# Kernel optimization log

Measured on AMD Instinct MI355X. Metric: run time of the kernel, lower is better.

Reference implementation:

```python
import jax, jax.numpy as jnp
import numpy as np
import math

N = 30000        # nodes
E = 390000       # edges (first N are self-loops, in node order)
H = 64
NNS = 4          # num_node_states
NES = 4          # num_edge_states
NGRAPH = 64      # graphs in batch
TEMP_ON_EVAL = 1.0


def from_binary(bits):
    # bits: [..., k] of {0,1} -> integer code sum(bits * 2^k)
    pw = (2 ** jnp.arange(bits.shape[-1])).astype(bits.dtype)
    return jnp.sum(bits * pw, axis=-1)


def segment_softmax(logits, seg, num_seg, tau):
    m = jax.ops.segment_max(logits, seg, num_segments=num_seg)
    e = jnp.exp((logits - m[seg]) / tau)
    s = jax.ops.segment_sum(e, seg, num_segments=num_seg)
    return e / s[seg]


def segment_hard_onehot(logits, seg, num_seg):
    # gumbel_softmax with tau=0, no noise: one-hot at per-segment argmax (first on ties)
    n = logits.shape[0]
    m = jax.ops.segment_max(logits, seg, num_segments=num_seg)
    idx = jnp.where(logits >= m[seg], jnp.arange(n, dtype=jnp.int32), jnp.int32(n))
    first = jax.ops.segment_min(idx, seg, num_segments=num_seg)
    return (jnp.arange(n, dtype=jnp.int32) == first[seg]).astype(jnp.int32)


def select_best(emb, bits, scalars, index, num_index):
    # SelectBest with use_select_best=True. states are even ints < 2^(k+1);
    # unique((states, index)) groups == fused key states*num_index+index.
    states = 2 * from_binary(bits)
    key = states * num_index + index
    num_key = (2 ** (bits.shape[-1] + 1)) * num_index
    best = segment_hard_onehot(-scalars[:, 0], key, num_key)
    return emb[states + best]


def temp_by_step(step, upper, lower, num_iter, temp_on_eval):
    if step == -1:
        return temp_on_eval
    frac = min(float(step) / num_iter, 1.0)
    return upper + (lower - upper) * frac


def forward(node_states, edge_states, scalars, edge_index, batch_vec, rev_idx,
            emb_edge, emb_sbv, emb_sbr, emb_static,
            Wq, Wk, Wv, Wek, Wev, Wc, training_step):
    ei0, ei1 = edge_index[0], edge_index[1]
    # self-loop edges are the first N edges in node order ->
    # scalars[edge_index[0]==edge_index[1]] == scalars[:N]
    node_scalars = scalars[:N]                                   # [N,1]

    # select_best_from_virtual
    node_fts = select_best(emb_sbv, node_states, node_scalars, batch_vec, NGRAPH)  # [N,H]
    edge_fts = emb_edge[from_binary(edge_states)]                # [E,H]

    Q = node_fts @ Wq.T
    K = node_fts @ Wk.T
    V = node_fts @ Wv.T

    # combined_edge_KV
    sb = select_best(emb_sbr, node_states[ei0], scalars, ei1, N)  # [E,H]
    edge_K = sb @ Wek.T
    sender_s = node_scalars[ei0]                                  # [E,1]
    reciever_s = node_scalars[ei1]                                # [E,1]
    rlx = (scalars < reciever_s)
    rlx_d = (sender_s + scalars < reciever_s)
    fts = jnp.concatenate([rlx, rlx_d], axis=-1).astype(jnp.int32)  # [E,2] bits
    static_fts = emb_static[from_binary(fts)]                     # [E,H]
    combined = jnp.concatenate([edge_fts, edge_fts[rev_idx], static_fts], axis=1)  # [E,3H]
    edge_V = combined @ Wc.T                                      # [E,H]

    # compute_message
    Qe = Q[ei1]
    Ke = K[ei0] + edge_K
    Ve = V[ei0] + edge_V
    alpha = jnp.sum(Qe * Ke, axis=-1) / math.sqrt(H)              # [E]
    tau = temp_by_step(int(training_step), 3.0, 0.1, 10000, TEMP_ON_EVAL)
    alpha = segment_softmax(alpha, ei1, N, tau)
    message = Ve * alpha[:, None]                                  # [E,H]

    node_out = node_fts + jax.ops.segment_sum(message, ei1, num_segments=N)
    edge_out = edge_fts + message
    return node_out, edge_out


def setup_inputs() -> dict:
    key = jax.random.key(0)
    ks = jax.random.split(key, 16)
    node_states = jax.random.randint(ks[0], (N, NNS), 0, 2, dtype=jnp.int32)
    edge_states = jax.random.randint(ks[1], (E, NES), 0, 2, dtype=jnp.int32)
    scalars = jax.random.normal(ks[2], (E, 1), dtype=jnp.float32)
    loops = jnp.arange(N, dtype=jnp.int32)
    senders = jax.random.randint(ks[3], (E - N,), 0, N, dtype=jnp.int32)
    receivers = jax.random.randint(ks[4], (E - N,), 0, N, dtype=jnp.int32)
    edge_index = jnp.stack([jnp.concatenate([loops, senders]),
                            jnp.concatenate([loops, receivers])])  # [2,E]
    batch_vec = jnp.sort(jax.random.randint(ks[5], (N,), 0, NGRAPH, dtype=jnp.int32))
    rev_idx = jax.random.permutation(ks[6], E).astype(jnp.int32)
    s = 0.05
    return {
        'node_states': node_states, 'edge_states': edge_states, 'scalars': scalars,
        'edge_index': edge_index, 'batch_vec': batch_vec, 'rev_idx': rev_idx,
        'emb_edge': s * jax.random.normal(ks[7], (2 ** NES, H), dtype=jnp.float32),
        'emb_sbv': s * jax.random.normal(ks[8], (2 ** (NNS + 1), H), dtype=jnp.float32),
        'emb_sbr': s * jax.random.normal(ks[9], (2 ** (NNS + 1), H), dtype=jnp.float32),
        'emb_static': s * jax.random.normal(ks[10], (4, H), dtype=jnp.float32),
        'Wq': s * jax.random.normal(ks[11], (H, H), dtype=jnp.float32),
        'Wk': s * jax.random.normal(ks[12], (H, H), dtype=jnp.float32),
        'Wv': s * jax.random.normal(ks[13], (H, H), dtype=jnp.float32),
        'Wek': s * jax.random.normal(ks[14], (H, H), dtype=jnp.float32),
        'Wev': s * jax.random.normal(ks[15], (H, H), dtype=jnp.float32),
        'Wc': s * jax.random.normal(jax.random.fold_in(key, 99), (H, 3 * H), dtype=jnp.float32),
        'training_step': -1,
    }


def reference(node_states, edge_states, scalars, edge_index, batch_vec, rev_idx,
              emb_edge, emb_sbv, emb_sbr, emb_static,
              Wq, Wk, Wv, Wek, Wev, Wc, training_step):
    return forward(node_states, edge_states, scalars, edge_index, batch_vec, rev_idx,
                   emb_edge, emb_sbv, emb_sbr, emb_static,
                   Wq, Wk, Wv, Wek, Wev, Wc, training_step)
```

## Files before the change

kernel.cpp:

```cpp
#include <hip/hip_runtime.h>

#define NN 30000
#define NE 390000
#define HH 64
#define NGRAPH 64
#define AGG_BLOCKS 1024
#define NE_BLK 1524
#define NN_BLK 118

__device__ __forceinline__ unsigned sortable_f32(float f) {
    unsigned u = __float_as_uint(f);
    return (u & 0x80000000u) ? ~u : (u | 0x80000000u);
}

#define T_V   0
#define T_C1  2048
#define T_C2  3072
#define T_C3  4096
#define T_A   4352
#define T_B   5376
#define T_Q   6400
#define T_K   8448
#define T_EK  10496

__global__ __launch_bounds__(256) void k_init(
        const int4* __restrict__ edge_states, const int4* __restrict__ node_states,
        const float* __restrict__ emb_sbv, const float* __restrict__ emb_sbr,
        const float* __restrict__ emb_edge, const float* __restrict__ emb_static,
        const float* __restrict__ Wq, const float* __restrict__ Wk,
        const float* __restrict__ Wv, const float* __restrict__ Wek,
        const float* __restrict__ Wc,
        unsigned char* __restrict__ esi, int* __restrict__ ns,
        unsigned* __restrict__ cnt, unsigned long long* __restrict__ nodeSel,
        float* __restrict__ tabs) {
    int b = blockIdx.x, t = threadIdx.x;
    if (b < NE_BLK) {
        int e = b * 256 + t;
        if (e < NE) {
            int4 v = edge_states[e];
            esi[e] = (unsigned char)(v.x + 2*v.y + 4*v.z + 8*v.w);
        }
    } else if (b < NE_BLK + NN_BLK) {
        int i = (b - NE_BLK) * 256 + t;
        if (i < NN) {
            int4 v = node_states[i];
            ns[i] = 2 * (v.x + 2*v.y + 4*v.z + 8*v.w);
            cnt[i] = 0u;
        }
    } else if (b < NE_BLK + NN_BLK + 41) {
        int idx = (b - NE_BLK - NN_BLK) * 256 + t;
        if (idx >= 10496) return;
        float acc = 0.f;
        if (idx < 2048) {
            int r = idx >> 6, h = idx & 63;
            for (int j = 0; j < 64; ++j) acc += emb_sbv[r*64+j] * Wv[h*64+j];
            tabs[T_V + idx] = acc;
        } else if (idx < 3072) {
            int x = idx - 2048; int r = x >> 6, h = x & 63;
            for (int j = 0; j < 64; ++j) acc += emb_edge[r*64+j] * Wc[h*192+j];
            tabs[T_C1 + x] = acc;
        } else if (idx < 4096) {
            int x = idx - 3072; int r = x >> 6, h = x & 63;
            for (int j = 0; j < 64; ++j) acc += emb_edge[r*64+j] * Wc[h*192+64+j];
            tabs[T_C2 + x] = acc;
        } else if (idx < 4352) {
            int x = idx - 4096; int r = x >> 6, h = x & 63;
            for (int j = 0; j < 64; ++j) acc += emb_static[r*64+j] * Wc[h*192+128+j];
            tabs[T_C3 + x] = acc;
        } else if (idx < 6400) {
            int x = idx - 4352; int r = x >> 6, h = x & 63;
            for (int j = 0; j < 64; ++j) acc += emb_sbv[r*64+j] * Wq[h*64+j];
            tabs[T_Q + x] = acc;
        } else if (idx < 8448) {
            int x = idx - 6400; int r = x >> 6, h = x & 63;
            for (int j = 0; j < 64; ++j) acc += emb_sbv[r*64+j] * Wk[h*64+j];
            tabs[T_K + x] = acc;
        } else {
            int x = idx - 8448; int r = x >> 6, h = x & 63;
            for (int j = 0; j < 64; ++j) acc += emb_sbr[r*64+j] * Wek[h*64+j];
            tabs[T_EK + x] = acc;
        }
    } else {
        #pragma unroll
        for (int k = 0; k < 4; ++k) nodeSel[t * 4 + k] = ~0ull;
    }
}

__global__ __launch_bounds__(256) void k_phase2(
        const int* __restrict__ ei1, unsigned* __restrict__ cnt,
        unsigned* __restrict__ rank, const int* __restrict__ ns,
        const int* __restrict__ batch_vec, const float* __restrict__ scalars,
        unsigned long long* __restrict__ nodeSel, float* __restrict__ tabs) {
    int b = blockIdx.x, t = threadIdx.x;
    if (b < NE_BLK) {
        int e = b * 256 + t;
        if (e < NE) rank[e] = atomicAdd(&cnt[ei1[e]], 1u);
    } else if (b < NE_BLK + NN_BLK) {
        int i = (b - NE_BLK) * 256 + t;
        if (i < NN) {
            int st = ns[i];
            int key = (st >> 1) * NGRAPH + batch_vec[i];
            unsigned long long pk = ((unsigned long long)sortable_f32(scalars[i]) << 32) | (unsigned)i;
            atomicMin(&nodeSel[key], pk);
        }
    } else {
        int idx = (b - NE_BLK - NN_BLK) * 256 + t;
        if (idx >= 2048) return;
        const float* TQ = tabs + T_Q;
        float acc = 0.f;
        if (idx < 1024) {
            int r1 = idx >> 5, r0 = idx & 31;
            const float* TK = tabs + T_K;
            for (int j = 0; j < 64; ++j) acc += TQ[r1*64+j] * TK[r0*64+j];
            tabs[T_A + idx] = acc * 0.125f;
        } else {
            int x = idx - 1024; int r1 = x >> 5, rk = x & 31;
            const float* TEK = tabs + T_EK;
            for (int j = 0; j < 64; ++j) acc += TQ[r1*64+j] * TEK[rk*64+j];
            tabs[T_B + x] = acc * 0.125f;
        }
    }
}

__global__ __launch_bounds__(256) void k_phase3(
        const unsigned* __restrict__ cnt, unsigned* __restrict__ bsum,
        const int* __restrict__ ns, const int* __restrict__ batch_vec,
        const unsigned long long* __restrict__ nodeSel,
        const float* __restrict__ scalars, uint2* __restrict__ nodePk) {
    int b = blockIdx.x, t = threadIdx.x;
    if (b < NN_BLK) {
        __shared__ unsigned red[256];
        int i = b * 256 + t;
        red[t] = (i < NN) ? cnt[i] : 0u;
        __syncthreads();
        for (int o = 128; o > 0; o >>= 1) {
            if (t < o) red[t] += red[t + o];
            __syncthreads();
        }
        if (t == 0) bsum[b] = red[0];
    } else {
        int i = (b - NN_BLK) * 256 + t;
        if (i < NN) {
            int st = ns[i];
            int key = (st >> 1) * NGRAPH + batch_vec[i];
            unsigned win = (unsigned)(nodeSel[key] & 0xffffffffull);
            unsigned row = (unsigned)st + (win == (unsigned)i ? 1u : 0u);
            nodePk[i] = make_uint2(row, __float_as_uint(scalars[i]));
        }
    }
}

__global__ __launch_bounds__(128) void k_sscan(const unsigned* __restrict__ bsum,
                                               unsigned* __restrict__ bbase,
                                               unsigned* __restrict__ base) {
    __shared__ unsigned s[128];
    int t = threadIdx.x;
    unsigned v = (t < NN_BLK) ? bsum[t] : 0u;
    s[t] = v;
    __syncthreads();
    for (int o = 1; o < 128; o <<= 1) {
        unsigned u = (t >= o) ? s[t - o] : 0u;
        __syncthreads();
        s[t] += u;
        __syncthreads();
    }
    if (t < NN_BLK) bbase[t] = s[t] - v;
    if (t == 127) { bbase[NN_BLK] = s[127]; base[NN] = s[127]; }
}

__global__ __launch_bounds__(256) void k_base(const unsigned* __restrict__ cnt,
        const unsigned* __restrict__ bbase, unsigned* __restrict__ base) {
    __shared__ unsigned s[256];
    int t = threadIdx.x;
    int i = blockIdx.x * 256 + t;
    unsigned v = (i < NN) ? cnt[i] : 0u;
    s[t] = v;
    __syncthreads();
    for (int o = 1; o < 256; o <<= 1) {
        unsigned u = (t >= o) ? s[t - o] : 0u;
        __syncthreads();
        s[t] += u;
        __syncthreads();
    }
    if (i < NN) base[i] = bbase[blockIdx.x] + s[t] - v;
}

__global__ __launch_bounds__(256) void k_edge2(const int* __restrict__ ei0,
        const int* __restrict__ ei1, const uint2* __restrict__ nodePk,
        const unsigned char* __restrict__ esi, const int* __restrict__ rev_idx,
        const float* __restrict__ scalars, const unsigned* __restrict__ base,
        const unsigned* __restrict__ rank, uint2* __restrict__ sKey,
        float* __restrict__ sScal) {
    int e = blockIdx.x * 256 + threadIdx.x;
    if (e >= NE) return;
    int s0 = ei0[e], s1 = ei1[e];
    uint2 np = nodePk[s0];
    unsigned es = esi[e];
    unsigned esr = esi[rev_idx[e]];
    unsigned pos = base[s1] + rank[e];
    sKey[pos] = make_uint2((unsigned)e | (np.x << 19) | (es << 24) | (esr << 28), np.y);
    sScal[pos] = scalars[e];
}

__global__ __launch_bounds__(256) void k_agg(
        const unsigned* __restrict__ base, const uint2* __restrict__ sKey,
        const float* __restrict__ sScal, const uint2* __restrict__ nodePk,
        const float* __restrict__ tabs, const float* __restrict__ emb_edge,
        const float* __restrict__ emb_sbv, const int* __restrict__ step_ptr,
        float* __restrict__ out_node, float* __restrict__ out_edge) {
    __shared__ float lds[9472];
    __shared__ unsigned scr[4][32];
    int tid = threadIdx.x;
    for (int j = tid; j < 6400; j += 256) lds[j] = tabs[j];
    for (int j = tid; j < 1024; j += 256) lds[6400 + j] = emb_edge[j];
    for (int j = tid; j < 2048; j += 256) lds[7424 + j] = emb_sbv[j];
    __syncthreads();
    int step = step_ptr[0];
    float invTau;
    if (step == -1) invTau = 1.0f;
    else { float frac = fminf((float)step / 10000.f, 1.f); invTau = 1.0f / (3.0f + (0.1f - 3.0f) * frac); }
    int wid = tid >> 6, lane = tid & 63;
    unsigned* mySc = scr[wid];
    unsigned* myE  = scr[wid] + 16;
    int q = lane >> 4, cidx = (lane & 15) << 2;
    for (int i = blockIdx.x * 4 + wid; i < NN; i += AGG_BLOCKS * 4) {
        unsigned j0 = base[i], j1 = base[i + 1];
        int d = (int)(j1 - j0);
        uint2 np = nodePk[i];
        int r1 = (int)np.x;
        float recv = __uint_as_float(np.y);
        const float* Arow = lds + T_A + r1 * 32;
        const float* Brow = lds + T_B + r1 * 32;
        float4 acc = {0.f, 0.f, 0.f, 0.f};
        if (lane < 16) { mySc[lane] = 0xffffffffu; myE[lane] = 0xffffffffu; }
        __builtin_amdgcn_sched_barrier(0);
        if (d > 0 && d <= 64) {
            bool act = lane < d;
            uint2 key = act ? sKey[j0 + lane] : make_uint2(0u, 0u);
            float sc  = act ? sScal[j0 + lane] : 0.f;
            unsigned scs = sortable_f32(sc);
            unsigned g = (key.x >> 20) & 15u;
            unsigned e19 = key.x & 0x7ffffu;
            if (act) atomicMin(&mySc[g], scs);
            __builtin_amdgcn_sched_barrier(0);
            unsigned ms = mySc[g];
            if (act && scs == ms) atomicMin(&myE[g], e19);
            __builtin_amdgcn_sched_barrier(0);
            bool win = act && (myE[g] == e19);
            int r0 = (key.x >> 19) & 31;
            int ekrow = (r0 & 30) + (win ? 1 : 0);
            float ex = act ? __expf((Arow[r0] + Brow[ekrow]) * invTau) : 0.f;
            float send = __uint_as_float(key.y);
            int si = (sc < recv ? 1 : 0) + (send + sc < recv ? 2 : 0);
            float s = ex;
            #pragma unroll
            for (int o = 1; o < 64; o <<= 1) s += __shfl_xor(s, o);
            float p = ex / s;
            int nIt = (d + 3) >> 2;
            for (int it = 0; it < nIt; ++it) {
                int jj = it * 4 + q;
                unsigned kx = __shfl(key.x, jj);
                int sii = __shfl(si, jj);
                float pp = __shfl(p, jj);
                if (jj < d) {
                    unsigned e = kx & 0x7ffffu;
                    int rr0 = (kx >> 19) & 31, es = (kx >> 24) & 15, esr = (kx >> 28) & 15;
                    float4 tv = *(const float4*)&lds[(rr0 << 6) + cidx];
                    float4 c1 = *(const float4*)&lds[T_C1 + (es << 6) + cidx];
                    float4 c2 = *(const float4*)&lds[T_C2 + (esr << 6) + cidx];
                    float4 c3 = *(const float4*)&lds[T_C3 + (sii << 6) + cidx];
                    float4 ee = *(const float4*)&lds[6400 + (es << 6) + cidx];
                    float4 o;
                    o.x = pp * (tv.x + c1.x + c2.x + c3.x);
                    o.y = pp * (tv.y + c1.y + c2.y + c3.y);
                    o.z = pp * (tv.z + c1.z + c2.z + c3.z);
                    o.w = pp * (tv.w + c1.w + c2.w + c3.w);
                    acc.x += o.x; acc.y += o.y; acc.z += o.z; acc.w += o.w;
                    o.x += ee.x; o.y += ee.y; o.z += ee.z; o.w += ee.w;
                    *(float4*)&out_edge[(size_t)e * 64 + cidx] = o;
                }
            }
        } else if (d > 64) {
            for (unsigned c = j0; c < j1; c += 64) {
                unsigned j = c + lane;
                if (j < j1) {
                    uint2 key = sKey[j];
                    atomicMin(&mySc[(key.x >> 20) & 15u], sortable_f32(sScal[j]));
                }
            }
            __builtin_amdgcn_sched_barrier(0);
            for (unsigned c = j0; c < j1; c += 64) {
                unsigned j = c + lane;
                if (j < j1) {
                    uint2 key = sKey[j];
                    unsigned g = (key.x >> 20) & 15u;
                    if (sortable_f32(sScal[j]) == mySc[g]) atomicMin(&myE[g], key.x & 0x7ffffu);
                }
            }
            __builtin_amdgcn_sched_barrier(0);
            float s = 0.f;
            for (unsigned c = j0; c < j1; c += 64) {
                unsigned j = c + lane;
                if (j < j1) {
                    uint2 key = sKey[j];
                    bool win = (myE[(key.x >> 20) & 15u] == (key.x & 0x7ffffu));
                    int r0 = (key.x >> 19) & 31;
                    int ekrow = (r0 & 30) + (win ? 1 : 0);
                    s += __expf((Arow[r0] + Brow[ekrow]) * invTau);
                }
            }
            #pragma unroll
            for (int o = 1; o < 64; o <<= 1) s += __shfl_xor(s, o);
            float invS = 1.f / s;
            for (unsigned c = j0; c < j1; c += 4) {
                unsigned j = c + q;
                if (j < j1) {
                    uint2 key = sKey[j];
                    float sc = sScal[j];
                    bool win = (myE[(key.x >> 20) & 15u] == (key.x & 0x7ffffu));
                    int r0 = (key.x >> 19) & 31;
                    int ekrow = (r0 & 30) + (win ? 1 : 0);
                    float pp = __expf((Arow[r0] + Brow[ekrow]) * invTau) * invS;
                    float send = __uint_as_float(key.y);
                    int si = (sc < recv ? 1 : 0) + (send + sc < recv ? 2 : 0);
                    unsigned e = key.x & 0x7ffffu;
                    int es = (key.x >> 24) & 15, esr = (key.x >> 28) & 15;
                    float4 tv = *(const float4*)&lds[(r0 << 6) + cidx];
                    float4 c1 = *(const float4*)&lds[T_C1 + (es << 6) + cidx];
                    float4 c2 = *(const float4*)&lds[T_C2 + (esr << 6) + cidx];
                    float4 c3 = *(const float4*)&lds[T_C3 + (si << 6) + cidx];
                    float4 ee = *(const float4*)&lds[6400 + (es << 6) + cidx];
                    float4 o;
                    o.x = pp * (tv.x + c1.x + c2.x + c3.x);
                    o.y = pp * (tv.y + c1.y + c2.y + c3.y);
                    o.z = pp * (tv.z + c1.z + c2.z + c3.z);
                    o.w = pp * (tv.w + c1.w + c2.w + c3.w);
                    acc.x += o.x; acc.y += o.y; acc.z += o.z; acc.w += o.w;
                    o.x += ee.x; o.y += ee.y; o.z += ee.z; o.w += ee.w;
                    *(float4*)&out_edge[(size_t)e * 64 + cidx] = o;
                }
            }
        }
        acc.x += __shfl_xor(acc.x, 16); acc.y += __shfl_xor(acc.y, 16);
        acc.z += __shfl_xor(acc.z, 16); acc.w += __shfl_xor(acc.w, 16);
        acc.x += __shfl_xor(acc.x, 32); acc.y += __shfl_xor(acc.y, 32);
        acc.z += __shfl_xor(acc.z, 32); acc.w += __shfl_xor(acc.w, 32);
        if (lane < 16) {
            float4 nb = *(const float4*)&lds[7424 + (r1 << 6) + cidx];
            float4 o;
            o.x = nb.x + acc.x; o.y = nb.y + acc.y; o.z = nb.z + acc.z; o.w = nb.w + acc.w;
            *(float4*)&out_node[(size_t)i * 64 + cidx] = o;
        }
    }
}

extern "C" void kernel_launch(void* const* d_in, const int* in_sizes, int n_in,
                              void* d_out, int out_size, void* d_ws, size_t ws_size,
                              hipStream_t stream) {
    const int4*  node_states = (const int4*)d_in[0];
    const int4*  edge_states = (const int4*)d_in[1];
    const float* scalars     = (const float*)d_in[2];
    const int*   edge_index  = (const int*)d_in[3];
    const int*   batch_vec   = (const int*)d_in[4];
    const int*   rev_idx     = (const int*)d_in[5];
    const float* emb_edge    = (const float*)d_in[6];
    const float* emb_sbv     = (const float*)d_in[7];
    const float* emb_sbr     = (const float*)d_in[8];
    const float* emb_static  = (const float*)d_in[9];
    const float* Wq  = (const float*)d_in[10];
    const float* Wk  = (const float*)d_in[11];
    const float* Wv  = (const float*)d_in[12];
    const float* Wek = (const float*)d_in[13];
    const float* Wc  = (const float*)d_in[15];
    const int*   step = (const int*)d_in[16];

    const int* ei0 = edge_index;
    const int* ei1 = edge_index + NE;

    char* ws = (char*)d_ws;
    int*      ns     = (int*)(ws);
    uint2*    nodePk = (uint2*)(ws + 120000);
    unsigned char* esi = (unsigned char*)(ws + 360000);
    unsigned* rank   = (unsigned*)(ws + 750016);
    unsigned* cnt    = (unsigned*)(ws + 2310016);
    unsigned* baseA  = (unsigned*)(ws + 2430080);
    uint2*    sKey   = (uint2*)(ws + 2550144);
    float*    sScal  = (float*)(ws + 5670144);
    unsigned long long* nodeSel = (unsigned long long*)(ws + 7230144);
    float*    tabs   = (float*)(ws + 7238336);
    unsigned* bsum   = (unsigned*)(ws + 7288512);
    unsigned* bbase  = (unsigned*)(ws + 7289024);

    float* out_node = (float*)d_out;
    float* out_edge = out_node + (size_t)NN * HH;

    hipLaunchKernelGGL(k_init, dim3(NE_BLK + NN_BLK + 41 + 1), dim3(256), 0, stream,
                       edge_states, node_states, emb_sbv, emb_sbr, emb_edge, emb_static,
                       Wq, Wk, Wv, Wek, Wc, esi, ns, cnt, nodeSel, tabs);
    hipLaunchKernelGGL(k_phase2, dim3(NE_BLK + NN_BLK + 8), dim3(256), 0, stream,
                       ei1, cnt, rank, ns, batch_vec, scalars, nodeSel, tabs);
    hipLaunchKernelGGL(k_phase3, dim3(NN_BLK * 2), dim3(256), 0, stream,
                       cnt, bsum, ns, batch_vec, nodeSel, scalars, nodePk);
    hipLaunchKernelGGL(k_sscan, dim3(1), dim3(128), 0, stream, bsum, bbase, baseA);
    hipLaunchKernelGGL(k_base, dim3(NN_BLK), dim3(256), 0, stream, cnt, bbase, baseA);
    hipLaunchKernelGGL(k_edge2, dim3(NE_BLK), dim3(256), 0, stream,
                       ei0, ei1, nodePk, esi, rev_idx, scalars, baseA, rank, sKey, sScal);
    hipLaunchKernelGGL(k_agg, dim3(AGG_BLOCKS), dim3(256), 0, stream,
                       baseA, sKey, sScal, nodePk, tabs, emb_edge, emb_sbv, step,
                       out_node, out_edge);
}
```

Before: 77.44 us.

## Fuse CSR scan kernels, pack edge payload, single 64-bit argmin atomic

Replaces the three-kernel block-sum/scan/base pipeline with one kernel in which each block recomputes its own prefix by summing all earlier counts, removing two launches. Edge key, sender scalar and edge scalar are packed into one 16-byte record, so aggregation issues one load per edge. The two-pass per-group argmin (min scalar, then min edge id) becomes a single 64-bit atomicMin on a packed (scalar, id) value. emb_sbv is read from global memory instead of LDS to shrink shared memory, and the aggregation grid grows. The trade-off is redundant prefix reads in later scan blocks and a wider payload with a padding word.

```diff
diff --git a/kernel.cpp b/kernel.cpp
--- a/kernel.cpp
+++ b/kernel.cpp
@@ -4,7 +4,7 @@
 #define NE 390000
 #define HH 64
 #define NGRAPH 64
-#define AGG_BLOCKS 1024
+#define AGG_BLOCKS 1536
 #define NE_BLK 1524
 #define NN_BLK 118
 
@@ -122,22 +122,37 @@
     }
 }
 
-__global__ __launch_bounds__(256) void k_phase3(
-        const unsigned* __restrict__ cnt, unsigned* __restrict__ bsum,
+__global__ __launch_bounds__(256) void k_csr(
+        const unsigned* __restrict__ cnt, unsigned* __restrict__ base,
         const int* __restrict__ ns, const int* __restrict__ batch_vec,
         const unsigned long long* __restrict__ nodeSel,
         const float* __restrict__ scalars, uint2* __restrict__ nodePk) {
     int b = blockIdx.x, t = threadIdx.x;
     if (b < NN_BLK) {
         __shared__ unsigned red[256];
-        int i = b * 256 + t;
-        red[t] = (i < NN) ? cnt[i] : 0u;
+        __shared__ unsigned sc[256];
+        unsigned pre = 0;
+        int lim = b * 256;
+        for (int j = t; j < lim; j += 256) pre += cnt[j];
+        red[t] = pre;
         __syncthreads();
         for (int o = 128; o > 0; o >>= 1) {
             if (t < o) red[t] += red[t + o];
             __syncthreads();
         }
-        if (t == 0) bsum[b] = red[0];
+        unsigned P = red[0];
+        int i = lim + t;
+        unsigned v = (i < NN) ? cnt[i] : 0u;
+        sc[t] = v;
+        __syncthreads();
+        for (int o = 1; o < 256; o <<= 1) {
+            unsigned u = (t >= o) ? sc[t - o] : 0u;
+            __syncthreads();
+            sc[t] += u;
+            __syncthreads();
+        }
+        if (i < NN) base[i] = P + sc[t] - v;
+        if (b == NN_BLK - 1 && t == 255) base[NN] = P + sc[255];
     } else {
         int i = (b - NN_BLK) * 256 + t;
         if (i < NN) {
@@ -150,47 +165,11 @@
     }
 }
 
-__global__ __launch_bounds__(128) void k_sscan(const unsigned* __restrict__ bsum,
-                                               unsigned* __restrict__ bbase,
-                                               unsigned* __restrict__ base) {
-    __shared__ unsigned s[128];
-    int t = threadIdx.x;
-    unsigned v = (t < NN_BLK) ? bsum[t] : 0u;
-    s[t] = v;
-    __syncthreads();
-    for (int o = 1; o < 128; o <<= 1) {
-        unsigned u = (t >= o) ? s[t - o] : 0u;
-        __syncthreads();
-        s[t] += u;
-        __syncthreads();
-    }
-    if (t < NN_BLK) bbase[t] = s[t] - v;
-    if (t == 127) { bbase[NN_BLK] = s[127]; base[NN] = s[127]; }
-}
-
-__global__ __launch_bounds__(256) void k_base(const unsigned* __restrict__ cnt,
-        const unsigned* __restrict__ bbase, unsigned* __restrict__ base) {
-    __shared__ unsigned s[256];
-    int t = threadIdx.x;
-    int i = blockIdx.x * 256 + t;
-    unsigned v = (i < NN) ? cnt[i] : 0u;
-    s[t] = v;
-    __syncthreads();
-    for (int o = 1; o < 256; o <<= 1) {
-        unsigned u = (t >= o) ? s[t - o] : 0u;
-        __syncthreads();
-        s[t] += u;
-        __syncthreads();
-    }
-    if (i < NN) base[i] = bbase[blockIdx.x] + s[t] - v;
-}
-
 __global__ __launch_bounds__(256) void k_edge2(const int* __restrict__ ei0,
         const int* __restrict__ ei1, const uint2* __restrict__ nodePk,
         const unsigned char* __restrict__ esi, const int* __restrict__ rev_idx,
         const float* __restrict__ scalars, const unsigned* __restrict__ base,
-        const unsigned* __restrict__ rank, uint2* __restrict__ sKey,
-        float* __restrict__ sScal) {
+        const unsigned* __restrict__ rank, uint4* __restrict__ sPay) {
     int e = blockIdx.x * 256 + threadIdx.x;
     if (e >= NE) return;
     int s0 = ei0[e], s1 = ei1[e];
@@ -198,30 +177,28 @@
     unsigned es = esi[e];
     unsigned esr = esi[rev_idx[e]];
     unsigned pos = base[s1] + rank[e];
-    sKey[pos] = make_uint2((unsigned)e | (np.x << 19) | (es << 24) | (esr << 28), np.y);
-    sScal[pos] = scalars[e];
+    sPay[pos] = make_uint4((unsigned)e | (np.x << 19) | (es << 24) | (esr << 28),
+                           np.y, __float_as_uint(scalars[e]), 0u);
 }
 
 __global__ __launch_bounds__(256) void k_agg(
-        const unsigned* __restrict__ base, const uint2* __restrict__ sKey,
-        const float* __restrict__ sScal, const uint2* __restrict__ nodePk,
-        const float* __restrict__ tabs, const float* __restrict__ emb_edge,
-        const float* __restrict__ emb_sbv, const int* __restrict__ step_ptr,
+        const unsigned* __restrict__ base, const uint4* __restrict__ sPay,
+        const uint2* __restrict__ nodePk, const float* __restrict__ tabs,
+        const float* __restrict__ emb_edge, const float* __restrict__ emb_sbv,
+        const int* __restrict__ step_ptr,
         float* __restrict__ out_node, float* __restrict__ out_edge) {
-    __shared__ float lds[9472];
-    __shared__ unsigned scr[4][32];
+    __shared__ float lds[7424];
+    __shared__ unsigned long long scr[4][16];
     int tid = threadIdx.x;
     for (int j = tid; j < 6400; j += 256) lds[j] = tabs[j];
     for (int j = tid; j < 1024; j += 256) lds[6400 + j] = emb_edge[j];
-    for (int j = tid; j < 2048; j += 256) lds[7424 + j] = emb_sbv[j];
     __syncthreads();
     int step = step_ptr[0];
     float invTau;
     if (step == -1) invTau = 1.0f;
     else { float frac = fminf((float)step / 10000.f, 1.f); invTau = 1.0f / (3.0f + (0.1f - 3.0f) * frac); }
     int wid = tid >> 6, lane = tid & 63;
-    unsigned* mySc = scr[wid];
-    unsigned* myE  = scr[wid] + 16;
+    unsigned long long* myPk = scr[wid];
     int q = lane >> 4, cidx = (lane & 15) << 2;
     for (int i = blockIdx.x * 4 + wid; i < NN; i += AGG_BLOCKS * 4) {
         unsigned j0 = base[i], j1 = base[i + 1];
@@ -232,25 +209,22 @@
         const float* Arow = lds + T_A + r1 * 32;
         const float* Brow = lds + T_B + r1 * 32;
         float4 acc = {0.f, 0.f, 0.f, 0.f};
-        if (lane < 16) { mySc[lane] = 0xffffffffu; myE[lane] = 0xffffffffu; }
+        if (lane < 16) myPk[lane] = ~0ull;
         __builtin_amdgcn_sched_barrier(0);
         if (d > 0 && d <= 64) {
             bool act = lane < d;
-            uint2 key = act ? sKey[j0 + lane] : make_uint2(0u, 0u);
-            float sc  = act ? sScal[j0 + lane] : 0.f;
-            unsigned scs = sortable_f32(sc);
-            unsigned g = (key.x >> 20) & 15u;
-            unsigned e19 = key.x & 0x7ffffu;
-            if (act) atomicMin(&mySc[g], scs);
+            uint4 pay = act ? sPay[j0 + lane] : make_uint4(0u, 0u, 0u, 0u);
+            float sc  = __uint_as_float(pay.z);
+            unsigned g = (pay.x >> 20) & 15u;
+            unsigned e19 = pay.x & 0x7ffffu;
+            unsigned long long pk = ((unsigned long long)sortable_f32(sc) << 32) | e19;
+            if (act) atomicMin(&myPk[g], pk);
             __builtin_amdgcn_sched_barrier(0);
-            unsigned ms = mySc[g];
-            if (act && scs == ms) atomicMin(&myE[g], e19);
-            __builtin_amdgcn_sched_barrier(0);
-            bool win = act && (myE[g] == e19);
-            int r0 = (key.x >> 19) & 31;
+            bool win = act && (myPk[g] == pk);
+            int r0 = (pay.x >> 19) & 31;
             int ekrow = (r0 & 30) + (win ? 1 : 0);
             float ex = act ? __expf((Arow[r0] + Brow[ekrow]) * invTau) : 0.f;
-            float send = __uint_as_float(key.y);
+            float send = __uint_as_float(pay.y);
             int si = (sc < recv ? 1 : 0) + (send + sc < recv ? 2 : 0);
             float s = ex;
             #pragma unroll
@@ -259,7 +233,7 @@
             int nIt = (d + 3) >> 2;
             for (int it = 0; it < nIt; ++it) {
                 int jj = it * 4 + q;
-                unsigned kx = __shfl(key.x, jj);
+                unsigned kx = __shfl(pay.x, jj);
                 int sii = __shfl(si, jj);
                 float pp = __shfl(p, jj);
                 if (jj < d) {
@@ -284,17 +258,11 @@
             for (unsigned c = j0; c < j1; c += 64) {
                 unsigned j = c + lane;
                 if (j < j1) {
-                    uint2 key = sKey[j];
-                    atomicMin(&mySc[(key.x >> 20) & 15u], sortable_f32(sScal[j]));
-                }
-            }
-            __builtin_amdgcn_sched_barrier(0);
-            for (unsigned c = j0; c < j1; c += 64) {
-                unsigned j = c + lane;
-                if (j < j1) {
-                    uint2 key = sKey[j];
-                    unsigned g = (key.x >> 20) & 15u;
-                    if (sortable_f32(sScal[j]) == mySc[g]) atomicMin(&myE[g], key.x & 0x7ffffu);
+                    uint4 pay = sPay[j];
+                    unsigned long long pk =
+                        ((unsigned long long)sortable_f32(__uint_as_float(pay.z)) << 32)
+                        | (pay.x & 0x7ffffu);
+                    atomicMin(&myPk[(pay.x >> 20) & 15u], pk);
                 }
             }
             __builtin_amdgcn_sched_barrier(0);
@@ -302,9 +270,12 @@
             for (unsigned c = j0; c < j1; c += 64) {
                 unsigned j = c + lane;
                 if (j < j1) {
-                    uint2 key = sKey[j];
-                    bool win = (myE[(key.x >> 20) & 15u] == (key.x & 0x7ffffu));
-                    int r0 = (key.x >> 19) & 31;
+                    uint4 pay = sPay[j];
+                    unsigned long long pk =
+                        ((unsigned long long)sortable_f32(__uint_as_float(pay.z)) << 32)
+                        | (pay.x & 0x7ffffu);
+                    bool win = (myPk[(pay.x >> 20) & 15u] == pk);
+                    int r0 = (pay.x >> 19) & 31;
                     int ekrow = (r0 & 30) + (win ? 1 : 0);
                     s += __expf((Arow[r0] + Brow[ekrow]) * invTau);
                 }
@@ -315,16 +286,18 @@
             for (unsigned c = j0; c < j1; c += 4) {
                 unsigned j = c + q;
                 if (j < j1) {
-                    uint2 key = sKey[j];
-                    float sc = sScal[j];
-                    bool win = (myE[(key.x >> 20) & 15u] == (key.x & 0x7ffffu));
-                    int r0 = (key.x >> 19) & 31;
+                    uint4 pay = sPay[j];
+                    float sc = __uint_as_float(pay.z);
+                    unsigned long long pk =
+                        ((unsigned long long)sortable_f32(sc) << 32) | (pay.x & 0x7ffffu);
+                    bool win = (myPk[(pay.x >> 20) & 15u] == pk);
+                    int r0 = (pay.x >> 19) & 31;
                     int ekrow = (r0 & 30) + (win ? 1 : 0);
                     float pp = __expf((Arow[r0] + Brow[ekrow]) * invTau) * invS;
-                    float send = __uint_as_float(key.y);
+                    float send = __uint_as_float(pay.y);
                     int si = (sc < recv ? 1 : 0) + (send + sc < recv ? 2 : 0);
-                    unsigned e = key.x & 0x7ffffu;
-                    int es = (key.x >> 24) & 15, esr = (key.x >> 28) & 15;
+                    unsigned e = pay.x & 0x7ffffu;
+                    int es = (pay.x >> 24) & 15, esr = (pay.x >> 28) & 15;
                     float4 tv = *(const float4*)&lds[(r0 << 6) + cidx];
                     float4 c1 = *(const float4*)&lds[T_C1 + (es << 6) + cidx];
                     float4 c2 = *(const float4*)&lds[T_C2 + (esr << 6) + cidx];
@@ -346,7 +319,7 @@
         acc.x += __shfl_xor(acc.x, 32); acc.y += __shfl_xor(acc.y, 32);
         acc.z += __shfl_xor(acc.z, 32); acc.w += __shfl_xor(acc.w, 32);
         if (lane < 16) {
-            float4 nb = *(const float4*)&lds[7424 + (r1 << 6) + cidx];
+            float4 nb = *(const float4*)&emb_sbv[(r1 << 6) + cidx];
             float4 o;
             o.x = nb.x + acc.x; o.y = nb.y + acc.y; o.z = nb.z + acc.z; o.w = nb.w + acc.w;
             *(float4*)&out_node[(size_t)i * 64 + cidx] = o;
@@ -384,12 +357,9 @@
     unsigned* rank   = (unsigned*)(ws + 750016);
     unsigned* cnt    = (unsigned*)(ws + 2310016);
     unsigned* baseA  = (unsigned*)(ws + 2430080);
-    uint2*    sKey   = (uint2*)(ws + 2550144);
-    float*    sScal  = (float*)(ws + 5670144);
-    unsigned long long* nodeSel = (unsigned long long*)(ws + 7230144);
-    float*    tabs   = (float*)(ws + 7238336);
-    unsigned* bsum   = (unsigned*)(ws + 7288512);
-    unsigned* bbase  = (unsigned*)(ws + 7289024);
+    uint4*    sPay   = (uint4*)(ws + 2550144);
+    unsigned long long* nodeSel = (unsigned long long*)(ws + 8790144);
+    float*    tabs   = (float*)(ws + 8798336);
 
     float* out_node = (float*)d_out;
     float* out_edge = out_node + (size_t)NN * HH;
@@ -399,13 +369,11 @@
                        Wq, Wk, Wv, Wek, Wc, esi, ns, cnt, nodeSel, tabs);
     hipLaunchKernelGGL(k_phase2, dim3(NE_BLK + NN_BLK + 8), dim3(256), 0, stream,
                        ei1, cnt, rank, ns, batch_vec, scalars, nodeSel, tabs);
-    hipLaunchKernelGGL(k_phase3, dim3(NN_BLK * 2), dim3(256), 0, stream,
-                       cnt, bsum, ns, batch_vec, nodeSel, scalars, nodePk);
-    hipLaunchKernelGGL(k_sscan, dim3(1), dim3(128), 0, stream, bsum, bbase, baseA);
-    hipLaunchKernelGGL(k_base, dim3(NN_BLK), dim3(256), 0, stream, cnt, bbase, baseA);
+    hipLaunchKernelGGL(k_csr, dim3(NN_BLK * 2), dim3(256), 0, stream,
+                       cnt, baseA, ns, batch_vec, nodeSel, scalars, nodePk);
     hipLaunchKernelGGL(k_edge2, dim3(NE_BLK), dim3(256), 0, stream,
-                       ei0, ei1, nodePk, esi, rev_idx, scalars, baseA, rank, sKey, sScal);
+                       ei0, ei1, nodePk, esi, rev_idx, scalars, baseA, rank, sPay);
     hipLaunchKernelGGL(k_agg, dim3(AGG_BLOCKS), dim3(256), 0, stream,
-                       baseA, sKey, sScal, nodePk, tabs, emb_edge, emb_sbv, step,
+                       baseA, sPay, nodePk, tabs, emb_edge, emb_sbv, step,
                        out_node, out_edge);
 }
```

New measurement: 91.90 us. 18.7% more time.
